# Optimization experiments

Hardware: AMD Instinct MI355X
Metric: run time of the kernel (lower is better)

## Reference

```python
import jax, jax.numpy as jnp
import numpy as np

BETA = 0.25


def setup_inputs() -> dict:
    key = jax.random.key(0)
    k1, k2 = jax.random.split(key)
    x = jax.random.normal(k1, (64, 32, 32, 64), dtype=jnp.float32)
    # codebook stored as [embedding_dim, num_embeddings], as in the layer
    embeddings = jax.random.normal(k2, (64, 1024), dtype=jnp.float32) * 0.05
    return {"x": x, "embeddings": embeddings}


def reference(x, embeddings):
    input_shape = x.shape
    d = embeddings.shape[0]
    flat = x.reshape(-1, d)  # [N, D]

    sim = flat @ embeddings  # [N, K]
    distances = (
        jnp.sum(flat ** 2, axis=1, keepdims=True)
        + jnp.sum(embeddings ** 2, axis=0)
        - 2.0 * sim
    )
    encoding_indices = jnp.argmin(distances, axis=1)  # [N]

    # one_hot @ embeddings.T is mathematically a gather of codebook rows
    quantized = jnp.take(embeddings.T, encoding_indices, axis=0)  # [N, D]
    quantized = quantized.reshape(input_shape)

    commitment_loss = jnp.mean((jax.lax.stop_gradient(quantized) - x) ** 2)
    codebook_loss = jnp.mean((quantized - jax.lax.stop_gradient(x)) ** 2)
    loss = BETA * commitment_loss + codebook_loss

    # straight-through estimator
    quantized_st = x + jax.lax.stop_gradient(quantized - x)
    return quantized_st, loss
```

## Files before the change

### kernel.cpp

```cpp
#include <hip/hip_runtime.h>

#define D 64
#define K 1024
#define NPTS 65536
#define OUT_ELEMS (NPTS * D)

typedef _Float16 f16x8 __attribute__((ext_vector_type(8)));
typedef float    f32x4 __attribute__((ext_vector_type(4)));

#define SCL  4096.0f
#define ISCL 0.000244140625f


static __device__ __forceinline__ void split16(float v, _Float16& h, _Float16& ls) {
    h = (_Float16)v;
    const float r = (v - (float)h) * SCL;
    ls = (_Float16)r;
}

__global__ __launch_bounds__(256) void vq_prep(const float* __restrict__ emb,
                                               float* __restrict__ eT,
                                               float* __restrict__ enorm_h,
                                               _Float16* __restrict__ ehf,
                                               _Float16* __restrict__ elf,
                                               float* __restrict__ loss_out) {
    __shared__ float tile[64][65];
    const int t    = threadIdx.x;
    const int lane = t & 63;
    const int quad = t >> 6;
    const int k0   = blockIdx.x * 64;

#pragma unroll
    for (int i = 0; i < 16; ++i) {
        const int d = i * 4 + quad;
        tile[d][lane] = emb[d * K + k0 + lane];
    }
    __syncthreads();

    const int kk = t >> 2, c = t & 3;
    const int krow = k0 + kk;
    const int ct   = krow >> 4, col = krow & 15;
#pragma unroll
    for (int j = 0; j < 16; ++j) {
        const int d = c * 16 + j;
        const float v = tile[d][kk];
        eT[krow * D + d] = v;
        _Float16 h, ls;
        split16(v, h, ls);
        const int off = ((ct * 2 + (d >> 5)) * 64 + ((d >> 3) & 3) * 16 + col) * 8
                        + (d & 7);
        ehf[off] = h; elf[off] = ls;
    }

    if (t < 64) {
        float s = __fmul_rn(tile[0][t], tile[0][t]);
        for (int dd = 1; dd < D; ++dd)
            s = __fadd_rn(s, __fmul_rn(tile[dd][t], tile[dd][t]));
        enorm_h[k0 + t] = 0.5f * s;
    }
    if (blockIdx.x == 0 && t == 0) *loss_out = 0.0f;
}

static __device__ __forceinline__ float sq8(float a, float b, float c, float d,
                                            float e, float f, float g, float h) {
    float r = __fmul_rn(a, a);
    r = __fadd_rn(r, __fmul_rn(b, b));
    r = __fadd_rn(r, __fmul_rn(c, c));
    r = __fadd_rn(r, __fmul_rn(d, d));
    r = __fadd_rn(r, __fmul_rn(e, e));
    r = __fadd_rn(r, __fmul_rn(f, f));
    r = __fadd_rn(r, __fmul_rn(g, g));
    r = __fadd_rn(r, __fmul_rn(h, h));
    return r;
}

#define PINF(v) asm volatile("" : "+v"(v))

#define MFMA(A, B, C) C = __builtin_amdgcn_mfma_f32_16x16x32_f16(A, B, C, 0, 0, 0)

#define MKFRAG16(FH, FS, U0, U1) {                        \
    _Float16 h_, s_;                                      \
    split16(U0.x, h_, s_); FH[0]=h_; FS[0]=s_;            \
    split16(U0.y, h_, s_); FH[1]=h_; FS[1]=s_;            \
    split16(U0.z, h_, s_); FH[2]=h_; FS[2]=s_;            \
    split16(U0.w, h_, s_); FH[3]=h_; FS[3]=s_;            \
    split16(U1.x, h_, s_); FH[4]=h_; FS[4]=s_;            \
    split16(U1.y, h_, s_); FH[5]=h_; FS[5]=s_;            \
    split16(U1.z, h_, s_); FH[6]=h_; FS[6]=s_;            \
    split16(U1.w, h_, s_); FH[7]=h_; FS[7]=s_; }

__global__ __launch_bounds__(512, 4) void vq_main(const float* __restrict__ x,
        const float* __restrict__ eT, const float* __restrict__ enorm_h,
        const _Float16* __restrict__ ehf, const _Float16* __restrict__ elf,
        float* __restrict__ out, float* __restrict__ loss_out) {
    __shared__ __align__(16) char smem[38400];
    float* rpart = (float*)smem;
    int*   swin  = (int*)(smem + 4096);
    float* skey  = (float*)(smem + 4608);
    int*   sct   = (int*)(smem + 21504);

    const int t     = threadIdx.x;
    const int lane  = t & 63;
    const int w     = t >> 6;
    const int m     = lane & 15;
    const int quad  = lane >> 4;
    const int g     = w >> 1;
    const int h     = w & 1;
    const int pbase = blockIdx.x * 128 + g * 32;

    f16x8 Ah00, As00, Ah01, As01;
    f16x8 Ah10, As10, Ah11, As11;
#define LOADA(TT, HH, FH, FS) {                                            \
    const float* px = x + ((size_t)(pbase + TT * 16 + m)) * D + HH * 32 + quad * 8; \
    const float4 u0 = *(const float4*)px;                                  \
    const float4 u1 = *(const float4*)(px + 4);                            \
    if (h == 0)                                                            \
        rpart[(g * 32 + TT * 16 + m) * 8 + (HH * 4 + quad)] =              \
            sq8(u0.x, u0.y, u0.z, u0.w, u1.x, u1.y, u1.z, u1.w);           \
    MKFRAG16(FH, FS, u0, u1); }
    LOADA(0, 0, Ah00, As00)
    LOADA(0, 1, Ah01, As01)
    LOADA(1, 0, Ah10, As10)
    LOADA(1, 1, Ah11, As11)
#undef LOADA
    PINF(Ah00); PINF(As00); PINF(Ah01); PINF(As01);
    PINF(Ah10); PINF(As10); PINF(Ah11); PINF(As11);

    const float FINF = 3.402823466e38f;
    float bk00 = FINF, bk01 = FINF, bk02 = FINF, bk03 = FINF;
    float bk10 = FINF, bk11 = FINF, bk12 = FINF, bk13 = FINF;
    int   bc00 = 0, bc01 = 0, bc02 = 0, bc03 = 0;
    int   bc10 = 0, bc11 = 0, bc12 = 0, bc13 = 0;

    const char* bh = (const char*)ehf + (size_t)h * 65536 + (size_t)lane * 16;
    const char* bs = (const char*)elf + (size_t)h * 65536 + (size_t)lane * 16;
    const float* enp = enorm_h + h * 512 + m;

#define COMPUTE(CT, BH0, BH1, BS0, BS1, ENH) {                             \
    f32x4 m0a = {0.f,0.f,0.f,0.f}, m0b = {0.f,0.f,0.f,0.f};                \
    f32x4 c0a = {0.f,0.f,0.f,0.f}, c0b = {0.f,0.f,0.f,0.f};                \
    f32x4 m1a = {0.f,0.f,0.f,0.f}, m1b = {0.f,0.f,0.f,0.f};                \
    f32x4 c1a = {0.f,0.f,0.f,0.f}, c1b = {0.f,0.f,0.f,0.f};                \
    MFMA(Ah00, BH0, m0a); MFMA(Ah10, BH0, m1a);           \
    MFMA(Ah01, BH1, m0b); MFMA(Ah11, BH1, m1b);           \
    MFMA(As00, BH0, c0a); MFMA(As10, BH0, c1a);                \
    MFMA(As01, BH1, c0b); MFMA(As11, BH1, c1b);                            \
    MFMA(Ah00, BS0, c0a); MFMA(Ah10, BS0, c1a);                \
    MFMA(Ah01, BS1, c0b); MFMA(Ah11, BS1, c1b);                            \
    const f32x4 d0 = (m0a + m0b) + ISCL * (c0a + c0b);                     \
    const f32x4 d1 = (m1a + m1b) + ISCL * (c1a + c1b);                     \
    { const float kv = ENH - d0[0]; if (kv < bk00) { bk00 = kv; bc00 = (CT); } } \
    { const float kv = ENH - d0[1]; if (kv < bk01) { bk01 = kv; bc01 = (CT); } } \
    { const float kv = ENH - d0[2]; if (kv < bk02) { bk02 = kv; bc02 = (CT); } } \
    { const float kv = ENH - d0[3]; if (kv < bk03) { bk03 = kv; bc03 = (CT); } } \
    { const float kv = ENH - d1[0]; if (kv < bk10) { bk10 = kv; bc10 = (CT); } } \
    { const float kv = ENH - d1[1]; if (kv < bk11) { bk11 = kv; bc11 = (CT); } } \
    { const float kv = ENH - d1[2]; if (kv < bk12) { bk12 = kv; bc12 = (CT); } } \
    { const float kv = ENH - d1[3]; if (kv < bk13) { bk13 = kv; bc13 = (CT); } } }

#define LOADB(TT, BH0, BH1, BS0, BS1, ENH) {                               \
    const int ob_ = (TT) * 2048;                                           \
    BH0 = *(const f16x8*)(bh + ob_);        BH1 = *(const f16x8*)(bh + ob_ + 1024); \
    BS0 = *(const f16x8*)(bs + ob_);        BS1 = *(const f16x8*)(bs + ob_ + 1024); \
    ENH = enp[(TT) * 16]; }

    f16x8 aBh0, aBh1, aBs0, aBs1;  float aEn;
    f16x8 pBh0, pBh1, pBs0, pBs1;  float pEn;

    LOADB(0, aBh0, aBh1, aBs0, aBs1, aEn)
    for (int j = 0; j < 16; ++j) {
        const int t1 = 2 * j + 1;
        const int t2 = (2 * j + 2) & 31;
        LOADB(t1, pBh0, pBh1, pBs0, pBs1, pEn)
        COMPUTE(2 * j, aBh0, aBh1, aBs0, aBs1, aEn)
        LOADB(t2, aBh0, aBh1, aBs0, aBs1, aEn)
        COMPUTE(t1, pBh0, pBh1, pBs0, pBs1, pEn)
    }
#undef LOADB
#undef COMPUTE

#define PUTC(TT, REG, BK, BC) {                                   \
    const int ploc = g * 32 + TT * 16 + quad * 4 + REG;           \
    skey[ploc * 33 + h * 16 + m] = BK;                            \
    sct [ploc * 33 + h * 16 + m] = BC; }
    PUTC(0, 0, bk00, bc00) PUTC(0, 1, bk01, bc01)
    PUTC(0, 2, bk02, bc02) PUTC(0, 3, bk03, bc03)
    PUTC(1, 0, bk10, bc10) PUTC(1, 1, bk11, bc11)
    PUTC(1, 2, bk12, bc12) PUTC(1, 3, bk13, bc13)
#undef PUTC
    __syncthreads();

    if (t < 128) {
        const int p = t;
        const float* rp = rpart + p * 8;
        const float A = ((rp[0] + rp[1]) + (rp[2] + rp[3])) +
                        ((rp[4] + rp[5]) + (rp[6] + rp[7]));
        float fb = FINF;
        int   fi = 0;
#pragma unroll
        for (int c = 0; c < 32; ++c) {
            const float kv = skey[p * 33 + c];
            const int   iv = (c >> 4) * 512 + sct[p * 33 + c] * 16 + (c & 15);
            if (kv < fb || (kv == fb && iv < fi)) { fb = kv; fi = iv; }
        }
        swin[p] = fi;
        float lp = fmaf(2.0f, fb, A);
#pragma unroll
        for (int off = 32; off > 0; off >>= 1) lp += __shfl_down(lp, off, 64);
        if (lane == 0) atomicAdd(loss_out, lp * (1.25f / (float)OUT_ELEMS));
    }
    __syncthreads();

    {
        const float4* eT4 = (const float4*)eT;
        float4* og = (float4*)out + (size_t)blockIdx.x * 2048;
#pragma unroll
        for (int s = 0; s < 4; ++s) {
            const int f  = s * 512 + t;
            const int fi = swin[f >> 4];
            og[f] = eT4[(size_t)fi * 16 + (f & 15)];
        }
    }
}

extern "C" void kernel_launch(void* const* d_in, const int* in_sizes, int n_in,
                              void* d_out, int out_size, void* d_ws, size_t ws_size,
                              hipStream_t stream) {
    const float* x   = (const float*)d_in[0];
    const float* emb = (const float*)d_in[1];
    float* out       = (float*)d_out;
    char*  ws        = (char*)d_ws;
    float*    eT      = (float*)ws;
    float*    enorm_h = (float*)(ws + 262144);
    _Float16* ehf     = (_Float16*)(ws + 266240);
    _Float16* elf     = (_Float16*)(ws + 397312);
    float* loss_out   = out + OUT_ELEMS;

    vq_prep<<<dim3(K / 64), dim3(256), 0, stream>>>(emb, eT, enorm_h, ehf, elf,
                                                    loss_out);
    vq_main<<<dim3(NPTS / 128), dim3(512), 0, stream>>>(x, eT, enorm_h, ehf,
                                                        elf, out, loss_out);
}
```

Measured before the change: 108.0 us.

## Give each wave 64 points to reuse codebook fragments, reduce argmin via shuffles

Each wave now handles four 16-point tiles instead of two, so every codebook B fragment loaded from global memory feeds twice as many MFMAs, and the block shrinks to 256 threads. MFMA chains are restructured to accumulate across the K halves in place, and the low-part correction is folded into a single FMA per candidate. The per-point argmin over codebook columns moves from a 33-wide shared-memory scan to a cross-lane shuffle reduction, shrinking LDS use. The cost is roughly double the per-thread registers for A fragments and running minima, with occupancy lowered to 2 waves per SIMD by the launch bounds.

```diff
diff --git a/kernel.cpp b/kernel.cpp
--- a/kernel.cpp
+++ b/kernel.cpp
@@ -76,7 +76,7 @@
 
 #define PINF(v) asm volatile("" : "+v"(v))
 
-#define MFMA(A, B, C) C = __builtin_amdgcn_mfma_f32_16x16x32_f16(A, B, C, 0, 0, 0)
+#define MF(A, B, C) __builtin_amdgcn_mfma_f32_16x16x32_f16(A, B, C, 0, 0, 0)
 
 #define MKFRAG16(FH, FS, U0, U1) {                        \
     _Float16 h_, s_;                                      \
@@ -89,15 +89,15 @@
     split16(U1.z, h_, s_); FH[6]=h_; FS[6]=s_;            \
     split16(U1.w, h_, s_); FH[7]=h_; FS[7]=s_; }
 
-__global__ __launch_bounds__(512, 4) void vq_main(const float* __restrict__ x,
+__global__ __launch_bounds__(256, 2) void vq_main(const float* __restrict__ x,
         const float* __restrict__ eT, const float* __restrict__ enorm_h,
         const _Float16* __restrict__ ehf, const _Float16* __restrict__ elf,
         float* __restrict__ out, float* __restrict__ loss_out) {
-    __shared__ __align__(16) char smem[38400];
+    __shared__ __align__(16) char smem[6656];
     float* rpart = (float*)smem;
     int*   swin  = (int*)(smem + 4096);
-    float* skey  = (float*)(smem + 4608);
-    int*   sct   = (int*)(smem + 21504);
+    float* sbk   = (float*)(smem + 4608);
+    int*   sbi   = (int*)(smem + 5632);
 
     const int t     = threadIdx.x;
     const int lane  = t & 63;
@@ -106,57 +106,80 @@
     const int quad  = lane >> 4;
     const int g     = w >> 1;
     const int h     = w & 1;
-    const int pbase = blockIdx.x * 128 + g * 32;
-
-    f16x8 Ah00, As00, Ah01, As01;
-    f16x8 Ah10, As10, Ah11, As11;
+    const int pbase = blockIdx.x * 128 + g * 64;
+
+    f16x8 Ah0_0, Ah0_1, As0_0, As0_1;
+    f16x8 Ah1_0, Ah1_1, As1_0, As1_1;
+    f16x8 Ah2_0, Ah2_1, As2_0, As2_1;
+    f16x8 Ah3_0, Ah3_1, As3_0, As3_1;
 #define LOADA(TT, HH, FH, FS) {                                            \
     const float* px = x + ((size_t)(pbase + TT * 16 + m)) * D + HH * 32 + quad * 8; \
     const float4 u0 = *(const float4*)px;                                  \
     const float4 u1 = *(const float4*)(px + 4);                            \
     if (h == 0)                                                            \
-        rpart[(g * 32 + TT * 16 + m) * 8 + (HH * 4 + quad)] =              \
+        rpart[(g * 64 + TT * 16 + m) * 8 + (HH * 4 + quad)] =              \
             sq8(u0.x, u0.y, u0.z, u0.w, u1.x, u1.y, u1.z, u1.w);           \
     MKFRAG16(FH, FS, u0, u1); }
-    LOADA(0, 0, Ah00, As00)
-    LOADA(0, 1, Ah01, As01)
-    LOADA(1, 0, Ah10, As10)
-    LOADA(1, 1, Ah11, As11)
+    LOADA(0, 0, Ah0_0, As0_0)  LOADA(0, 1, Ah0_1, As0_1)
+    LOADA(1, 0, Ah1_0, As1_0)  LOADA(1, 1, Ah1_1, As1_1)
+    LOADA(2, 0, Ah2_0, As2_0)  LOADA(2, 1, Ah2_1, As2_1)
+    LOADA(3, 0, Ah3_0, As3_0)  LOADA(3, 1, Ah3_1, As3_1)
 #undef LOADA
-    PINF(Ah00); PINF(As00); PINF(Ah01); PINF(As01);
-    PINF(Ah10); PINF(As10); PINF(Ah11); PINF(As11);
+    PINF(Ah0_0); PINF(Ah0_1); PINF(As0_0); PINF(As0_1);
+    PINF(Ah1_0); PINF(Ah1_1); PINF(As1_0); PINF(As1_1);
+    PINF(Ah2_0); PINF(Ah2_1); PINF(As2_0); PINF(As2_1);
+    PINF(Ah3_0); PINF(Ah3_1); PINF(As3_0); PINF(As3_1);
+
+    f32x4 ZERO = {0.f, 0.f, 0.f, 0.f};
+    PINF(ZERO);
 
     const float FINF = 3.402823466e38f;
-    float bk00 = FINF, bk01 = FINF, bk02 = FINF, bk03 = FINF;
-    float bk10 = FINF, bk11 = FINF, bk12 = FINF, bk13 = FINF;
-    int   bc00 = 0, bc01 = 0, bc02 = 0, bc03 = 0;
-    int   bc10 = 0, bc11 = 0, bc12 = 0, bc13 = 0;
+    float bk0_0 = FINF, bk0_1 = FINF, bk0_2 = FINF, bk0_3 = FINF;
+    float bk1_0 = FINF, bk1_1 = FINF, bk1_2 = FINF, bk1_3 = FINF;
+    float bk2_0 = FINF, bk2_1 = FINF, bk2_2 = FINF, bk2_3 = FINF;
+    float bk3_0 = FINF, bk3_1 = FINF, bk3_2 = FINF, bk3_3 = FINF;
+    int   bc0_0 = 0, bc0_1 = 0, bc0_2 = 0, bc0_3 = 0;
+    int   bc1_0 = 0, bc1_1 = 0, bc1_2 = 0, bc1_3 = 0;
+    int   bc2_0 = 0, bc2_1 = 0, bc2_2 = 0, bc2_3 = 0;
+    int   bc3_0 = 0, bc3_1 = 0, bc3_2 = 0, bc3_3 = 0;
 
     const char* bh = (const char*)ehf + (size_t)h * 65536 + (size_t)lane * 16;
     const char* bs = (const char*)elf + (size_t)h * 65536 + (size_t)lane * 16;
     const float* enp = enorm_h + h * 512 + m;
 
+#define AC1(BK, BC, MV, CV, CT, ENH) {                                     \
+    const float kv = __builtin_fmaf(-ISCL, CV, (ENH) - (MV));              \
+    if (kv < BK) { BK = kv; BC = (CT); } }
+
 #define COMPUTE(CT, BH0, BH1, BS0, BS1, ENH) {                             \
-    f32x4 m0a = {0.f,0.f,0.f,0.f}, m0b = {0.f,0.f,0.f,0.f};                \
-    f32x4 c0a = {0.f,0.f,0.f,0.f}, c0b = {0.f,0.f,0.f,0.f};                \
-    f32x4 m1a = {0.f,0.f,0.f,0.f}, m1b = {0.f,0.f,0.f,0.f};                \
-    f32x4 c1a = {0.f,0.f,0.f,0.f}, c1b = {0.f,0.f,0.f,0.f};                \
-    MFMA(Ah00, BH0, m0a); MFMA(Ah10, BH0, m1a);           \
-    MFMA(Ah01, BH1, m0b); MFMA(Ah11, BH1, m1b);           \
-    MFMA(As00, BH0, c0a); MFMA(As10, BH0, c1a);                \
-    MFMA(As01, BH1, c0b); MFMA(As11, BH1, c1b);                            \
-    MFMA(Ah00, BS0, c0a); MFMA(Ah10, BS0, c1a);                \
-    MFMA(Ah01, BS1, c0b); MFMA(Ah11, BS1, c1b);                            \
-    const f32x4 d0 = (m0a + m0b) + ISCL * (c0a + c0b);                     \
-    const f32x4 d1 = (m1a + m1b) + ISCL * (c1a + c1b);                     \
-    { const float kv = ENH - d0[0]; if (kv < bk00) { bk00 = kv; bc00 = (CT); } } \
-    { const float kv = ENH - d0[1]; if (kv < bk01) { bk01 = kv; bc01 = (CT); } } \
-    { const float kv = ENH - d0[2]; if (kv < bk02) { bk02 = kv; bc02 = (CT); } } \
-    { const float kv = ENH - d0[3]; if (kv < bk03) { bk03 = kv; bc03 = (CT); } } \
-    { const float kv = ENH - d1[0]; if (kv < bk10) { bk10 = kv; bc10 = (CT); } } \
-    { const float kv = ENH - d1[1]; if (kv < bk11) { bk11 = kv; bc11 = (CT); } } \
-    { const float kv = ENH - d1[2]; if (kv < bk12) { bk12 = kv; bc12 = (CT); } } \
-    { const float kv = ENH - d1[3]; if (kv < bk13) { bk13 = kv; bc13 = (CT); } } }
+    f32x4 m0 = MF(Ah0_0, BH0, ZERO);  f32x4 m1 = MF(Ah1_0, BH0, ZERO);     \
+    f32x4 m2 = MF(Ah2_0, BH0, ZERO);  f32x4 m3 = MF(Ah3_0, BH0, ZERO);     \
+    f32x4 c0 = MF(As0_0, BH0, ZERO);  f32x4 c1 = MF(As1_0, BH0, ZERO);     \
+    f32x4 c2 = MF(As2_0, BH0, ZERO);  f32x4 c3 = MF(As3_0, BH0, ZERO);     \
+    m0 = MF(Ah0_1, BH1, m0);  m1 = MF(Ah1_1, BH1, m1);                     \
+    m2 = MF(Ah2_1, BH1, m2);  m3 = MF(Ah3_1, BH1, m3);                     \
+    c0 = MF(As0_1, BH1, c0);  c1 = MF(As1_1, BH1, c1);                     \
+    c2 = MF(As2_1, BH1, c2);  c3 = MF(As3_1, BH1, c3);                     \
+    c0 = MF(Ah0_0, BS0, c0);  c1 = MF(Ah1_0, BS0, c1);                     \
+    c2 = MF(Ah2_0, BS0, c2);  c3 = MF(Ah3_0, BS0, c3);                     \
+    c0 = MF(Ah0_1, BS1, c0);  c1 = MF(Ah1_1, BS1, c1);                     \
+    c2 = MF(Ah2_1, BS1, c2);  c3 = MF(Ah3_1, BS1, c3);                     \
+    AC1(bk0_0, bc0_0, m0[0], c0[0], CT, ENH)                               \
+    AC1(bk0_1, bc0_1, m0[1], c0[1], CT, ENH)                               \
+    AC1(bk0_2, bc0_2, m0[2], c0[2], CT, ENH)                               \
+    AC1(bk0_3, bc0_3, m0[3], c0[3], CT, ENH)                               \
+    AC1(bk1_0, bc1_0, m1[0], c1[0], CT, ENH)                               \
+    AC1(bk1_1, bc1_1, m1[1], c1[1], CT, ENH)                               \
+    AC1(bk1_2, bc1_2, m1[2], c1[2], CT, ENH)                               \
+    AC1(bk1_3, bc1_3, m1[3], c1[3], CT, ENH)                               \
+    AC1(bk2_0, bc2_0, m2[0], c2[0], CT, ENH)                               \
+    AC1(bk2_1, bc2_1, m2[1], c2[1], CT, ENH)                               \
+    AC1(bk2_2, bc2_2, m2[2], c2[2], CT, ENH)                               \
+    AC1(bk2_3, bc2_3, m2[3], c2[3], CT, ENH)                               \
+    AC1(bk3_0, bc3_0, m3[0], c3[0], CT, ENH)                               \
+    AC1(bk3_1, bc3_1, m3[1], c3[1], CT, ENH)                               \
+    AC1(bk3_2, bc3_2, m3[2], c3[2], CT, ENH)                               \
+    AC1(bk3_3, bc3_3, m3[3], c3[3], CT, ENH) }
 
 #define LOADB(TT, BH0, BH1, BS0, BS1, ENH) {                               \
     const int ob_ = (TT) * 2048;                                           \
@@ -178,16 +201,29 @@
     }
 #undef LOADB
 #undef COMPUTE
-
-#define PUTC(TT, REG, BK, BC) {                                   \
-    const int ploc = g * 32 + TT * 16 + quad * 4 + REG;           \
-    skey[ploc * 33 + h * 16 + m] = BK;                            \
-    sct [ploc * 33 + h * 16 + m] = BC; }
-    PUTC(0, 0, bk00, bc00) PUTC(0, 1, bk01, bc01)
-    PUTC(0, 2, bk02, bc02) PUTC(0, 3, bk03, bc03)
-    PUTC(1, 0, bk10, bc10) PUTC(1, 1, bk11, bc11)
-    PUTC(1, 2, bk12, bc12) PUTC(1, 3, bk13, bc13)
-#undef PUTC
+#undef AC1
+
+#define LEXSTEP(KV, IV, MSK) {                                             \
+    const float ok_ = __shfl_xor(KV, MSK, 64);                             \
+    const int   oi_ = __shfl_xor(IV, MSK, 64);                             \
+    if (ok_ < KV || (ok_ == KV && oi_ < IV)) { KV = ok_; IV = oi_; } }
+#define REDUCE1(BK, BC, TT, EE) {                                          \
+    float kv = BK; int iv = h * 512 + BC * 16 + m;                         \
+    LEXSTEP(kv, iv, 1) LEXSTEP(kv, iv, 2)                                  \
+    LEXSTEP(kv, iv, 4) LEXSTEP(kv, iv, 8)                                  \
+    if (m == 0) {                                                          \
+        const int p = g * 64 + (TT) * 16 + quad * 4 + (EE);                \
+        sbk[h * 128 + p] = kv; sbi[h * 128 + p] = iv; } }
+    REDUCE1(bk0_0, bc0_0, 0, 0) REDUCE1(bk0_1, bc0_1, 0, 1)
+    REDUCE1(bk0_2, bc0_2, 0, 2) REDUCE1(bk0_3, bc0_3, 0, 3)
+    REDUCE1(bk1_0, bc1_0, 1, 0) REDUCE1(bk1_1, bc1_1, 1, 1)
+    REDUCE1(bk1_2, bc1_2, 1, 2) REDUCE1(bk1_3, bc1_3, 1, 3)
+    REDUCE1(bk2_0, bc2_0, 2, 0) REDUCE1(bk2_1, bc2_1, 2, 1)
+    REDUCE1(bk2_2, bc2_2, 2, 2) REDUCE1(bk2_3, bc2_3, 2, 3)
+    REDUCE1(bk3_0, bc3_0, 3, 0) REDUCE1(bk3_1, bc3_1, 3, 1)
+    REDUCE1(bk3_2, bc3_2, 3, 2) REDUCE1(bk3_3, bc3_3, 3, 3)
+#undef REDUCE1
+#undef LEXSTEP
     __syncthreads();
 
     if (t < 128) {
@@ -195,14 +231,9 @@
         const float* rp = rpart + p * 8;
         const float A = ((rp[0] + rp[1]) + (rp[2] + rp[3])) +
                         ((rp[4] + rp[5]) + (rp[6] + rp[7]));
-        float fb = FINF;
-        int   fi = 0;
-#pragma unroll
-        for (int c = 0; c < 32; ++c) {
-            const float kv = skey[p * 33 + c];
-            const int   iv = (c >> 4) * 512 + sct[p * 33 + c] * 16 + (c & 15);
-            if (kv < fb || (kv == fb && iv < fi)) { fb = kv; fi = iv; }
-        }
+        float fb = sbk[p];        int fi = sbi[p];
+        const float k1 = sbk[128 + p]; const int i1 = sbi[128 + p];
+        if (k1 < fb || (k1 == fb && i1 < fi)) { fb = k1; fi = i1; }
         swin[p] = fi;
         float lp = fmaf(2.0f, fb, A);
 #pragma unroll
@@ -215,8 +246,8 @@
         const float4* eT4 = (const float4*)eT;
         float4* og = (float4*)out + (size_t)blockIdx.x * 2048;
 #pragma unroll
-        for (int s = 0; s < 4; ++s) {
-            const int f  = s * 512 + t;
+        for (int s = 0; s < 8; ++s) {
+            const int f  = s * 256 + t;
             const int fi = swin[f >> 4];
             og[f] = eT4[(size_t)fi * 16 + (f & 15)];
         }
@@ -238,6 +269,6 @@
 
     vq_prep<<<dim3(K / 64), dim3(256), 0, stream>>>(emb, eT, enorm_h, ehf, elf,
                                                     loss_out);
-    vq_main<<<dim3(NPTS / 128), dim3(512), 0, stream>>>(x, eT, enorm_h, ehf,
+    vq_main<<<dim3(NPTS / 128), dim3(256), 0, stream>>>(x, eT, enorm_h, ehf,
                                                         elf, out, loss_out);
 }
```

Measured after the change: 115.1 us. 6.6% more time.

## Software-pipeline MFMA batches against argmin updates and fold norm into accumulator

Applied to the files above, without the earlier changes.

Restructures the codebook loop so the MFMAs for the next tile are issued before the argmin comparisons of the previous tile, overlapping matrix-core latency with VALU compare/select work. It also chains MFMAs through accumulators instead of summing separate partials, seeding the accumulator with the negated codebook norm and using a single FMA for the low-part correction. This cuts VALU adds and hides MFMA latency, at the cost of more live accumulator registers and a changed summation order.

```diff
diff --git a/kernel.cpp b/kernel.cpp
--- a/kernel.cpp
+++ b/kernel.cpp
@@ -76,7 +76,7 @@
 
 #define PINF(v) asm volatile("" : "+v"(v))
 
-#define MFMA(A, B, C) C = __builtin_amdgcn_mfma_f32_16x16x32_f16(A, B, C, 0, 0, 0)
+#define MF(A, B, C) __builtin_amdgcn_mfma_f32_16x16x32_f16(A, B, C, 0, 0, 0)
 
 #define MKFRAG16(FH, FS, U0, U1) {                        \
     _Float16 h_, s_;                                      \
@@ -126,6 +126,9 @@
     PINF(Ah00); PINF(As00); PINF(Ah01); PINF(As01);
     PINF(Ah10); PINF(As10); PINF(Ah11); PINF(As11);
 
+    f32x4 ZERO = {0.f, 0.f, 0.f, 0.f};
+    PINF(ZERO);
+
     const float FINF = 3.402823466e38f;
     float bk00 = FINF, bk01 = FINF, bk02 = FINF, bk03 = FINF;
     float bk10 = FINF, bk11 = FINF, bk12 = FINF, bk13 = FINF;
@@ -136,27 +139,25 @@
     const char* bs = (const char*)elf + (size_t)h * 65536 + (size_t)lane * 16;
     const float* enp = enorm_h + h * 512 + m;
 
-#define COMPUTE(CT, BH0, BH1, BS0, BS1, ENH) {                             \
-    f32x4 m0a = {0.f,0.f,0.f,0.f}, m0b = {0.f,0.f,0.f,0.f};                \
-    f32x4 c0a = {0.f,0.f,0.f,0.f}, c0b = {0.f,0.f,0.f,0.f};                \
-    f32x4 m1a = {0.f,0.f,0.f,0.f}, m1b = {0.f,0.f,0.f,0.f};                \
-    f32x4 c1a = {0.f,0.f,0.f,0.f}, c1b = {0.f,0.f,0.f,0.f};                \
-    MFMA(Ah00, BH0, m0a); MFMA(Ah10, BH0, m1a);           \
-    MFMA(Ah01, BH1, m0b); MFMA(Ah11, BH1, m1b);           \
-    MFMA(As00, BH0, c0a); MFMA(As10, BH0, c1a);                \
-    MFMA(As01, BH1, c0b); MFMA(As11, BH1, c1b);                            \
-    MFMA(Ah00, BS0, c0a); MFMA(Ah10, BS0, c1a);                \
-    MFMA(Ah01, BS1, c0b); MFMA(Ah11, BS1, c1b);                            \
-    const f32x4 d0 = (m0a + m0b) + ISCL * (c0a + c0b);                     \
-    const f32x4 d1 = (m1a + m1b) + ISCL * (c1a + c1b);                     \
-    { const float kv = ENH - d0[0]; if (kv < bk00) { bk00 = kv; bc00 = (CT); } } \
-    { const float kv = ENH - d0[1]; if (kv < bk01) { bk01 = kv; bc01 = (CT); } } \
-    { const float kv = ENH - d0[2]; if (kv < bk02) { bk02 = kv; bc02 = (CT); } } \
-    { const float kv = ENH - d0[3]; if (kv < bk03) { bk03 = kv; bc03 = (CT); } } \
-    { const float kv = ENH - d1[0]; if (kv < bk10) { bk10 = kv; bc10 = (CT); } } \
-    { const float kv = ENH - d1[1]; if (kv < bk11) { bk11 = kv; bc11 = (CT); } } \
-    { const float kv = ENH - d1[2]; if (kv < bk12) { bk12 = kv; bc12 = (CT); } } \
-    { const float kv = ENH - d1[3]; if (kv < bk13) { bk13 = kv; bc13 = (CT); } } }
+#define MFMAS(BH0, BH1, BS0, BS1, ENH, M0, M1, C0, C1) {                   \
+    const float ne_ = -(ENH);                                              \
+    const f32x4 ce_ = {ne_, ne_, ne_, ne_};                                \
+    M0 = MF(Ah00, BH0, ce_);   M1 = MF(Ah10, BH0, ce_);                    \
+    C0 = MF(As00, BH0, ZERO);  C1 = MF(As10, BH0, ZERO);                   \
+    M0 = MF(Ah01, BH1, M0);    M1 = MF(Ah11, BH1, M1);                     \
+    C0 = MF(As01, BH1, C0);    C1 = MF(As11, BH1, C1);                     \
+    C0 = MF(Ah00, BS0, C0);    C1 = MF(Ah10, BS0, C1);                     \
+    C0 = MF(Ah01, BS1, C0);    C1 = MF(Ah11, BS1, C1); }
+
+#define AC1(BK, BC, MV, CV, CT) {                                          \
+    const float kv = __builtin_fmaf(-ISCL, CV, -(MV));                     \
+    if (kv < BK) { BK = kv; BC = (CT); } }
+
+#define ARGM(M0, M1, C0, C1, CT) {                                         \
+    AC1(bk00, bc00, M0[0], C0[0], CT)  AC1(bk01, bc01, M0[1], C0[1], CT)   \
+    AC1(bk02, bc02, M0[2], C0[2], CT)  AC1(bk03, bc03, M0[3], C0[3], CT)   \
+    AC1(bk10, bc10, M1[0], C1[0], CT)  AC1(bk11, bc11, M1[1], C1[1], CT)   \
+    AC1(bk12, bc12, M1[2], C1[2], CT)  AC1(bk13, bc13, M1[3], C1[3], CT) }
 
 #define LOADB(TT, BH0, BH1, BS0, BS1, ENH) {                               \
     const int ob_ = (TT) * 2048;                                           \
@@ -166,18 +167,33 @@
 
     f16x8 aBh0, aBh1, aBs0, aBs1;  float aEn;
     f16x8 pBh0, pBh1, pBs0, pBs1;  float pEn;
+    f32x4 mE0, mE1, cE0, cE1;
+    f32x4 mO0, mO1, cO0, cO1;
 
     LOADB(0, aBh0, aBh1, aBs0, aBs1, aEn)
-    for (int j = 0; j < 16; ++j) {
+    LOADB(1, pBh0, pBh1, pBs0, pBs1, pEn)
+    MFMAS(aBh0, aBh1, aBs0, aBs1, aEn, mE0, mE1, cE0, cE1)
+    LOADB(2, aBh0, aBh1, aBs0, aBs1, aEn)
+
+    for (int j = 0; j < 15; ++j) {
         const int t1 = 2 * j + 1;
-        const int t2 = (2 * j + 2) & 31;
-        LOADB(t1, pBh0, pBh1, pBs0, pBs1, pEn)
-        COMPUTE(2 * j, aBh0, aBh1, aBs0, aBs1, aEn)
-        LOADB(t2, aBh0, aBh1, aBs0, aBs1, aEn)
-        COMPUTE(t1, pBh0, pBh1, pBs0, pBs1, pEn)
-    }
+        const int t2 = 2 * j + 2;
+        const int t3 = 2 * j + 3;
+        const int t4 = (2 * j + 4) & 31;
+        MFMAS(pBh0, pBh1, pBs0, pBs1, pEn, mO0, mO1, cO0, cO1)
+        LOADB(t3, pBh0, pBh1, pBs0, pBs1, pEn)
+        ARGM(mE0, mE1, cE0, cE1, 2 * j)
+        MFMAS(aBh0, aBh1, aBs0, aBs1, aEn, mE0, mE1, cE0, cE1)
+        LOADB(t4, aBh0, aBh1, aBs0, aBs1, aEn)
+        ARGM(mO0, mO1, cO0, cO1, t1)
+    }
+    MFMAS(pBh0, pBh1, pBs0, pBs1, pEn, mO0, mO1, cO0, cO1)
+    ARGM(mE0, mE1, cE0, cE1, 30)
+    ARGM(mO0, mO1, cO0, cO1, 31)
 #undef LOADB
-#undef COMPUTE
+#undef ARGM
+#undef AC1
+#undef MFMAS
 
 #define PUTC(TT, REG, BK, BC) {                                   \
     const int ploc = g * 32 + TT * 16 + quad * 4 + REG;           \
```

Measured after the change: 122.1 us. 13.1% more time.

## Deepen codebook prefetch to triple-buffer, chain MFMA accumulators, pin A fragments to AGPRs

Applied to the files above, without the earlier changes.

The B-fragment prefetch goes from double to triple buffering, so each tile's loads are issued two compute steps ahead. MFMA accumulation now chains through fewer accumulators from a shared zero register, and the scale-and-subtract is folded into one fma per candidate. The A fragments and the zero vector are constrained to AGPRs, and s_setprio is raised around the MFMA block. This aims to hide global-load latency and cut VGPR pressure and VALU work. In exchange, the longer serial MFMA dependency chains may add latency, and the AGPR constraint could force extra moves.

```diff
diff --git a/kernel.cpp b/kernel.cpp
--- a/kernel.cpp
+++ b/kernel.cpp
@@ -74,9 +74,10 @@
     return r;
 }
 
-#define PINF(v) asm volatile("" : "+v"(v))
-
-#define MFMA(A, B, C) C = __builtin_amdgcn_mfma_f32_16x16x32_f16(A, B, C, 0, 0, 0)
+#define PINF(v)  asm volatile("" : "+v"(v))
+#define PINFA(v) asm volatile("" : "+a"(v))
+
+#define MF(A, B, C) __builtin_amdgcn_mfma_f32_16x16x32_f16(A, B, C, 0, 0, 0)
 
 #define MKFRAG16(FH, FS, U0, U1) {                        \
     _Float16 h_, s_;                                      \
@@ -123,8 +124,11 @@
     LOADA(1, 0, Ah10, As10)
     LOADA(1, 1, Ah11, As11)
 #undef LOADA
-    PINF(Ah00); PINF(As00); PINF(Ah01); PINF(As01);
-    PINF(Ah10); PINF(As10); PINF(Ah11); PINF(As11);
+    PINFA(Ah00); PINFA(As00); PINFA(Ah01); PINFA(As01);
+    PINFA(Ah10); PINFA(As10); PINFA(Ah11); PINFA(As11);
+
+    f32x4 ZERO = {0.f, 0.f, 0.f, 0.f};
+    PINFA(ZERO);
 
     const float FINF = 3.402823466e38f;
     float bk00 = FINF, bk01 = FINF, bk02 = FINF, bk03 = FINF;
@@ -136,48 +140,57 @@
     const char* bs = (const char*)elf + (size_t)h * 65536 + (size_t)lane * 16;
     const float* enp = enorm_h + h * 512 + m;
 
-#define COMPUTE(CT, BH0, BH1, BS0, BS1, ENH) {                             \
-    f32x4 m0a = {0.f,0.f,0.f,0.f}, m0b = {0.f,0.f,0.f,0.f};                \
-    f32x4 c0a = {0.f,0.f,0.f,0.f}, c0b = {0.f,0.f,0.f,0.f};                \
-    f32x4 m1a = {0.f,0.f,0.f,0.f}, m1b = {0.f,0.f,0.f,0.f};                \
-    f32x4 c1a = {0.f,0.f,0.f,0.f}, c1b = {0.f,0.f,0.f,0.f};                \
-    MFMA(Ah00, BH0, m0a); MFMA(Ah10, BH0, m1a);           \
-    MFMA(Ah01, BH1, m0b); MFMA(Ah11, BH1, m1b);           \
-    MFMA(As00, BH0, c0a); MFMA(As10, BH0, c1a);                \
-    MFMA(As01, BH1, c0b); MFMA(As11, BH1, c1b);                            \
-    MFMA(Ah00, BS0, c0a); MFMA(Ah10, BS0, c1a);                \
-    MFMA(Ah01, BS1, c0b); MFMA(Ah11, BS1, c1b);                            \
-    const f32x4 d0 = (m0a + m0b) + ISCL * (c0a + c0b);                     \
-    const f32x4 d1 = (m1a + m1b) + ISCL * (c1a + c1b);                     \
-    { const float kv = ENH - d0[0]; if (kv < bk00) { bk00 = kv; bc00 = (CT); } } \
-    { const float kv = ENH - d0[1]; if (kv < bk01) { bk01 = kv; bc01 = (CT); } } \
-    { const float kv = ENH - d0[2]; if (kv < bk02) { bk02 = kv; bc02 = (CT); } } \
-    { const float kv = ENH - d0[3]; if (kv < bk03) { bk03 = kv; bc03 = (CT); } } \
-    { const float kv = ENH - d1[0]; if (kv < bk10) { bk10 = kv; bc10 = (CT); } } \
-    { const float kv = ENH - d1[1]; if (kv < bk11) { bk11 = kv; bc11 = (CT); } } \
-    { const float kv = ENH - d1[2]; if (kv < bk12) { bk12 = kv; bc12 = (CT); } } \
-    { const float kv = ENH - d1[3]; if (kv < bk13) { bk13 = kv; bc13 = (CT); } } }
-
-#define LOADB(TT, BH0, BH1, BS0, BS1, ENH) {                               \
+#define AC1(BK, BC, MV, CV, CT, ENH) {                                     \
+    const float kv = __builtin_fmaf(-ISCL, CV, (ENH) - (MV));              \
+    if (kv < BK) { BK = kv; BC = (CT); } }
+
+#define COMPUTE(CT, BH0, BH1, BS0, BS1) {                                  \
+    const float enh_ = enp[(CT) * 16];      \
+    __builtin_amdgcn_s_setprio(1);                                         \
+    f32x4 m0 = MF(Ah00, BH0, ZERO);  f32x4 m1 = MF(Ah10, BH0, ZERO);       \
+    f32x4 c0 = MF(As00, BH0, ZERO);  f32x4 c1 = MF(As10, BH0, ZERO);       \
+    m0 = MF(Ah01, BH1, m0);  m1 = MF(Ah11, BH1, m1);                       \
+    c0 = MF(As01, BH1, c0);  c1 = MF(As11, BH1, c1);                       \
+    c0 = MF(Ah00, BS0, c0);  c1 = MF(Ah10, BS0, c1);                       \
+    c0 = MF(Ah01, BS1, c0);  c1 = MF(Ah11, BS1, c1);                       \
+    __builtin_amdgcn_s_setprio(0);                                         \
+    AC1(bk00, bc00, m0[0], c0[0], CT, enh_)                                \
+    AC1(bk01, bc01, m0[1], c0[1], CT, enh_)                                \
+    AC1(bk02, bc02, m0[2], c0[2], CT, enh_)                                \
+    AC1(bk03, bc03, m0[3], c0[3], CT, enh_)                                \
+    AC1(bk10, bc10, m1[0], c1[0], CT, enh_)                                \
+    AC1(bk11, bc11, m1[1], c1[1], CT, enh_)                                \
+    AC1(bk12, bc12, m1[2], c1[2], CT, enh_)                                \
+    AC1(bk13, bc13, m1[3], c1[3], CT, enh_) }
+
+#define LOADB(TT, BH0, BH1, BS0, BS1) {                                    \
     const int ob_ = (TT) * 2048;                                           \
-    BH0 = *(const f16x8*)(bh + ob_);        BH1 = *(const f16x8*)(bh + ob_ + 1024); \
-    BS0 = *(const f16x8*)(bs + ob_);        BS1 = *(const f16x8*)(bs + ob_ + 1024); \
-    ENH = enp[(TT) * 16]; }
-
-    f16x8 aBh0, aBh1, aBs0, aBs1;  float aEn;
-    f16x8 pBh0, pBh1, pBs0, pBs1;  float pEn;
-
-    LOADB(0, aBh0, aBh1, aBs0, aBs1, aEn)
-    for (int j = 0; j < 16; ++j) {
-        const int t1 = 2 * j + 1;
-        const int t2 = (2 * j + 2) & 31;
-        LOADB(t1, pBh0, pBh1, pBs0, pBs1, pEn)
-        COMPUTE(2 * j, aBh0, aBh1, aBs0, aBs1, aEn)
-        LOADB(t2, aBh0, aBh1, aBs0, aBs1, aEn)
-        COMPUTE(t1, pBh0, pBh1, pBs0, pBs1, pEn)
-    }
+    BH0 = *(const f16x8*)(bh + ob_);                                       \
+    BH1 = *(const f16x8*)(bh + ob_ + 1024);                                \
+    BS0 = *(const f16x8*)(bs + ob_);                                       \
+    BS1 = *(const f16x8*)(bs + ob_ + 1024); }
+
+    f16x8 aBh0, aBh1, aBs0, aBs1;
+    f16x8 bBh0, bBh1, bBs0, bBs1;
+    f16x8 cBh0, cBh1, cBs0, cBs1;
+
+    LOADB(0, aBh0, aBh1, aBs0, aBs1)
+    LOADB(1, bBh0, bBh1, bBs0, bBs1)
+    LOADB(2, cBh0, cBh1, cBs0, cBs1)
+
+    for (int j = 0; j < 30; j += 3) {
+        COMPUTE(j,     aBh0, aBh1, aBs0, aBs1)
+        LOADB((j + 3) & 31, aBh0, aBh1, aBs0, aBs1)
+        COMPUTE(j + 1, bBh0, bBh1, bBs0, bBs1)
+        LOADB((j + 4) & 31, bBh0, bBh1, bBs0, bBs1)
+        COMPUTE(j + 2, cBh0, cBh1, cBs0, cBs1)
+        LOADB((j + 5) & 31, cBh0, cBh1, cBs0, cBs1)
+    }
+    COMPUTE(30, aBh0, aBh1, aBs0, aBs1)
+    COMPUTE(31, bBh0, bBh1, bBs0, bBs1)
 #undef LOADB
 #undef COMPUTE
+#undef AC1
 
 #define PUTC(TT, REG, BK, BC) {                                   \
     const int ploc = g * 32 + TT * 16 + quad * 4 + REG;           \
```

Result: slower. 258.9 us (+139.7%).
